# Performance work log

Hardware: AMD Instinct MI355X
Metric: run time of the kernel (lower is better)

## Reference

```python
import jax, jax.numpy as jnp
import numpy as np

# Dimensions: batch B, window W (time features), nodes M, hidden HID, hops NLAYERS
B, W, M, HID, NLAYERS = 32, 168, 2048, 128, 6


def setup_inputs() -> dict:
    key = jax.random.key(0)
    ks = jax.random.split(key, 6)
    x = jax.random.normal(ks[0], (B, W, M), dtype=jnp.float32)
    # scale L so matrix powers L^k stay bounded (spectral radius < 1)
    L = jax.random.normal(ks[1], (M, M), dtype=jnp.float32) / (2.0 * np.float32(np.sqrt(M)))
    # stacked per-hop MLP params: linears[i]: W->HID, linears2[i]: HID->1
    W1 = jax.random.normal(ks[2], (NLAYERS + 1, HID, W), dtype=jnp.float32) / np.float32(np.sqrt(W))
    b1 = jax.random.normal(ks[3], (NLAYERS + 1, HID), dtype=jnp.float32) * 0.01
    W2 = jax.random.normal(ks[4], (NLAYERS + 1, HID), dtype=jnp.float32) / np.float32(np.sqrt(HID))
    b2 = jax.random.normal(ks[5], (NLAYERS + 1,), dtype=jnp.float32) * 0.01
    return {"x": x, "L": L, "W1": W1, "b1": b1, "W2": W2, "b2": b2}


def _hop_mlp(t, w1, bb1, w2, bb2):
    # t: [B, M, W] -> scalar score per node: Linear(W->HID), ReLU, Linear(HID->1)
    h = jax.nn.relu(jnp.einsum('bmw,hw->bmh', t, w1) + bb1)
    return jnp.einsum('bmh,h->bm', h, w2) + bb2


def reference(x, L, W1, b1, W2, b2):
    xt = jnp.swapaxes(x, 1, 2)  # [B, M, W] (x.transpose(2,1))
    s = _hop_mlp(xt, W1[0], b1[0], W2[0], b2[0])  # [B, M]
    P = L
    for i in range(1, NLAYERS + 1):
        # PP.expand + bmm == broadcasted matmul; never materialize [B,M,M]
        t = jnp.einsum('ij,bjw->biw', P, xt)  # [B, M, W]
        s = s + _hop_mlp(t, W1[i], b1[i], W2[i], b2[i])
        P = jnp.matmul(L, P)  # next graph power
    return s  # [B, M]; output_fun is None so no final nonlinearity
```

## Files before the change

### kernel.cpp

```cpp
#include <hip/hip_runtime.h>
#include <cstdint>
#include <cstddef>

typedef __bf16 bf16_t;
typedef __attribute__((ext_vector_type(8))) __bf16 bf16x8;
typedef __attribute__((ext_vector_type(4))) __bf16 bf16x4;
typedef __attribute__((ext_vector_type(4))) float floatx4;

#define NB 32
#define NW 168
#define NM 2048
#define NHID 128
#define NBW (NB * NW)

#define GLOAD_LDS16(g, l)                                          \
  __builtin_amdgcn_global_load_lds(                                \
      (const __attribute__((address_space(1))) void*)(g),          \
      (__attribute__((address_space(3))) void*)(l), 16, 0, 0)

__global__ void cast_bf16_kernel(const float* __restrict__ in, bf16_t* __restrict__ out, int n4) {
  int stride = gridDim.x * blockDim.x;
  for (int i = blockIdx.x * blockDim.x + threadIdx.x; i < n4; i += stride) {
    float4 v = ((const float4*)in)[i];
    bf16x4 o = {(bf16_t)v.x, (bf16_t)v.y, (bf16_t)v.z, (bf16_t)v.w};
    ((bf16x4*)out)[i] = o;
  }
}

__global__ void prep_x_kernel(const float* __restrict__ x, bf16_t* __restrict__ Xb,
                              bf16_t* __restrict__ XT) {
  __shared__ float tile[64][65];
  const int R = NBW, C = NM;
  int r0 = blockIdx.y * 64, c0 = blockIdx.x * 64;
  int t = threadIdx.x;
  int tr = t >> 4, tc4 = (t & 15) * 4;
#pragma unroll
  for (int p = 0; p < 4; ++p) {
    int row = p * 16 + tr;
    float4 v = *(const float4*)(x + (size_t)(r0 + row) * C + c0 + tc4);
    tile[row][tc4 + 0] = v.x;
    tile[row][tc4 + 1] = v.y;
    tile[row][tc4 + 2] = v.z;
    tile[row][tc4 + 3] = v.w;
    bf16x4 o = {(bf16_t)v.x, (bf16_t)v.y, (bf16_t)v.z, (bf16_t)v.w};
    *(bf16x4*)(Xb + (size_t)(r0 + row) * C + c0 + tc4) = o;
  }
  __syncthreads();
#pragma unroll
  for (int p = 0; p < 4; ++p) {
    int c = p * 16 + tr;
    bf16x4 o = {(bf16_t)tile[tc4 + 0][c], (bf16_t)tile[tc4 + 1][c],
                (bf16_t)tile[tc4 + 2][c], (bf16_t)tile[tc4 + 3][c]};
    *(bf16x4*)(XT + (size_t)(c0 + c) * R + r0 + tc4) = o;
  }
}

__global__ void gemm_nt_kernel(const bf16_t* __restrict__ A, const bf16_t* __restrict__ Bt,
                               bf16_t* __restrict__ C, bf16_t* __restrict__ Ct,
                               int K, int lda, int ldb, int ldc, int ldct, int write_c) {
  __shared__ bf16_t As[128 * 32];
  __shared__ bf16_t Bs[128 * 32];
  int tid = threadIdx.x;
  int m0 = blockIdx.y * 128, n0 = blockIdx.x * 128;
  int lane = tid & 63, wv = tid >> 6;
  int wm = wv >> 1, wn = wv & 1;
  int quad = lane >> 4, l15 = lane & 15;

  int p0 = wv * 128 + lane;
  int p1 = p0 + 64;
  int row0 = p0 >> 2, kc0 = (p0 & 3) ^ ((p0 >> 3) & 3);
  int row1 = p1 >> 2, kc1 = (p1 & 3) ^ ((p1 >> 3) & 3);
  const bf16_t* a0p = A + (size_t)(m0 + row0) * lda + kc0 * 8;
  const bf16_t* a1p = A + (size_t)(m0 + row1) * lda + kc1 * 8;
  const bf16_t* b0p = Bt + (size_t)(n0 + row0) * ldb + kc0 * 8;
  const bf16_t* b1p = Bt + (size_t)(n0 + row1) * ldb + kc1 * 8;
  bf16_t* As_d0 = As + (size_t)(wv * 128) * 8;
  bf16_t* As_d1 = As + (size_t)(wv * 128 + 64) * 8;
  bf16_t* Bs_d0 = Bs + (size_t)(wv * 128) * 8;
  bf16_t* Bs_d1 = Bs + (size_t)(wv * 128 + 64) * 8;

  int swz = (l15 >> 1) & 3;
  int kpos = (quad ^ swz) * 8;

  floatx4 zero4 = {0.f, 0.f, 0.f, 0.f};
  floatx4 acc[4][4];
#pragma unroll
  for (int mi = 0; mi < 4; ++mi)
#pragma unroll
    for (int ni = 0; ni < 4; ++ni) acc[mi][ni] = zero4;

  for (int kb = 0; kb < K; kb += 32) {
    GLOAD_LDS16(a0p + kb, As_d0);
    GLOAD_LDS16(a1p + kb, As_d1);
    GLOAD_LDS16(b0p + kb, Bs_d0);
    GLOAD_LDS16(b1p + kb, Bs_d1);
    __syncthreads();
    bf16x8 af[4], bf[4];
#pragma unroll
    for (int mi = 0; mi < 4; ++mi)
      af[mi] = *(const bf16x8*)(As + (wm * 64 + mi * 16 + l15) * 32 + kpos);
#pragma unroll
    for (int ni = 0; ni < 4; ++ni)
      bf[ni] = *(const bf16x8*)(Bs + (wn * 64 + ni * 16 + l15) * 32 + kpos);
#pragma unroll
    for (int mi = 0; mi < 4; ++mi)
#pragma unroll
      for (int ni = 0; ni < 4; ++ni)
        acc[mi][ni] = __builtin_amdgcn_mfma_f32_16x16x32_bf16(af[mi], bf[ni], acc[mi][ni], 0, 0, 0);
    __syncthreads();
  }
#pragma unroll
  for (int mi = 0; mi < 4; ++mi) {
#pragma unroll
    for (int ni = 0; ni < 4; ++ni) {
      int col = n0 + wn * 64 + ni * 16 + l15;
      int rowb = m0 + wm * 64 + mi * 16 + quad * 4;
      bf16x4 tv;
#pragma unroll
      for (int r = 0; r < 4; ++r) tv[r] = (bf16_t)acc[mi][ni][r];
      *(bf16x4*)(Ct + (size_t)col * ldct + rowb) = tv;
      if (write_c) {
#pragma unroll
        for (int r = 0; r < 4; ++r)
          C[(size_t)(rowb + r) * ldc + col] = tv[r];
      }
    }
  }
}

__global__ void mlp_score_kernel(const bf16_t* __restrict__ T, const bf16_t* __restrict__ W1b,
                                 const float* __restrict__ b1, const float* __restrict__ W2,
                                 const float* __restrict__ b2, float* __restrict__ out,
                                 int hop, int accumulate) {
  __shared__ bf16_t Bs[24 * 128 * 8];
  __shared__ float sred[4][64];
  const bf16_t* Wh = W1b + (size_t)hop * NHID * NW;
  const float* b1h = b1 + hop * NHID;
  const float* w2h = W2 + hop * NHID;
  int tid = threadIdx.x;
  int r0 = blockIdx.x * 128;
  int lane = tid & 63, wv = tid >> 6;
  int wm = wv >> 1, wn = wv & 1;
  int quad = lane >> 4, l15 = lane & 15;

  for (int c = 2688 + tid; c < 3072; c += 256) {
    int4 z = {0, 0, 0, 0};
    *(int4*)(Bs + (size_t)c * 8) = z;
  }
  for (int i = 0; i < 11; ++i) {
    int c = i * 256 + tid;
    if (c < 2688) {
      int kc = c >> 7;
      int h = (c & 127) ^ ((kc & 3) << 2);
      GLOAD_LDS16(Wh + (size_t)h * NW + kc * 8, Bs + (size_t)(i * 256 + wv * 64) * 8);
    }
  }

  const bf16_t* arow[4];
#pragma unroll
  for (int mi = 0; mi < 4; ++mi) {
    int R = r0 + wm * 64 + mi * 16 + l15;
    arow[mi] = T + (size_t)(R >> 5) * NBW + (size_t)(R & 31) * NW + quad * 8;
  }

  floatx4 zero4 = {0.f, 0.f, 0.f, 0.f};
  floatx4 acc[4][4];
#pragma unroll
  for (int mi = 0; mi < 4; ++mi)
#pragma unroll
    for (int ni = 0; ni < 4; ++ni) acc[mi][ni] = zero4;

  __syncthreads();

#pragma unroll
  for (int kb = 0; kb < 192; kb += 32) {
    int kc = (kb >> 3) + quad;
    bf16x8 af[4], bf[4];
#pragma unroll
    for (int mi = 0; mi < 4; ++mi)
      af[mi] = *(const bf16x8*)(arow[mi] + kb);
#pragma unroll
    for (int ni = 0; ni < 4; ++ni) {
      int hpos = (wn * 64 + ni * 16 + l15) ^ ((kc & 3) << 2);
      bf[ni] = *(const bf16x8*)(Bs + (size_t)(kc * 128 + hpos) * 8);
    }
#pragma unroll
    for (int mi = 0; mi < 4; ++mi)
#pragma unroll
      for (int ni = 0; ni < 4; ++ni)
        acc[mi][ni] = __builtin_amdgcn_mfma_f32_16x16x32_bf16(af[mi], bf[ni], acc[mi][ni], 0, 0, 0);
  }

  float part[4][4];
#pragma unroll
  for (int mi = 0; mi < 4; ++mi)
#pragma unroll
    for (int r = 0; r < 4; ++r) part[mi][r] = 0.f;
#pragma unroll
  for (int ni = 0; ni < 4; ++ni) {
    int col = wn * 64 + ni * 16 + l15;
    float b1v = b1h[col];
    float w2v = w2h[col];
#pragma unroll
    for (int mi = 0; mi < 4; ++mi)
#pragma unroll
      for (int r = 0; r < 4; ++r) {
        float h = acc[mi][ni][r] + b1v;
        h = h > 0.f ? h : 0.f;
        part[mi][r] += h * w2v;
      }
  }
#pragma unroll
  for (int off = 1; off < 16; off <<= 1)
#pragma unroll
    for (int mi = 0; mi < 4; ++mi)
#pragma unroll
      for (int r = 0; r < 4; ++r) part[mi][r] += __shfl_xor(part[mi][r], off);
  if (l15 == 0) {
#pragma unroll
    for (int mi = 0; mi < 4; ++mi)
#pragma unroll
      for (int r = 0; r < 4; ++r) sred[wv][mi * 16 + quad * 4 + r] = part[mi][r];
  }
  __syncthreads();
  if (tid < 128) {
    int half = tid >> 6;
    int lr = tid & 63;
    float v = sred[half * 2][lr] + sred[half * 2 + 1][lr] + b2[hop];
    int R = r0 + half * 64 + lr;
    int idx = (R & 31) * NM + (R >> 5);
    if (accumulate)
      out[idx] += v;
    else
      out[idx] = v;
  }
}

extern "C" void kernel_launch(void* const* d_in, const int* in_sizes, int n_in,
                              void* d_out, int out_size, void* d_ws, size_t ws_size,
                              hipStream_t stream) {
  const float* x = (const float*)d_in[0];
  const float* L = (const float*)d_in[1];
  const float* W1 = (const float*)d_in[2];
  const float* b1 = (const float*)d_in[3];
  const float* W2 = (const float*)d_in[4];
  const float* b2 = (const float*)d_in[5];
  float* out = (float*)d_out;

  char* ws = (char*)d_ws;
  size_t off = 0;
  auto walloc = [&](size_t bytes) -> void* {
    off = (off + 255) & ~(size_t)255;
    void* p = ws + off;
    off += bytes;
    return p;
  };
  bf16_t* Xb = (bf16_t*)walloc((size_t)NBW * NM * 2);
  bf16_t* XT = (bf16_t*)walloc((size_t)NM * NBW * 2);
  bf16_t* Lb = (bf16_t*)walloc((size_t)NM * NM * 2);
  bf16_t* W1b = (bf16_t*)walloc((size_t)7 * NHID * NW * 2);
  bf16_t* Ta = (bf16_t*)walloc((size_t)NBW * NM * 2);
  (void)ws_size; (void)in_sizes; (void)n_in; (void)out_size;

  prep_x_kernel<<<dim3(NM / 64, NBW / 64), dim3(256), 0, stream>>>(x, Xb, XT);
  cast_bf16_kernel<<<dim3(1024), dim3(256), 0, stream>>>(L, Lb, NM * NM / 4);
  cast_bf16_kernel<<<dim3(64), dim3(256), 0, stream>>>(W1, W1b, 7 * NHID * NW / 4);

  mlp_score_kernel<<<dim3(NM * NB / 128), dim3(256), 0, stream>>>(XT, W1b, b1, W2, b2, out, 0, 0);

  bf16_t* src = Xb;
  bf16_t* dst = Ta;
  for (int i = 1; i <= 6; ++i) {
    gemm_nt_kernel<<<dim3(NM / 128, NBW / 128), dim3(256), 0, stream>>>(
        src, Lb, dst, XT, NM, NM, NM, NM, NBW, (i < 6) ? 1 : 0);
    mlp_score_kernel<<<dim3(NM * NB / 128), dim3(256), 0, stream>>>(XT, W1b, b1, W2, b2, out, i, 1);
    bf16_t* t = src; src = dst; dst = t;
  }
}
```

Measured before the change: 553.3 us.

## Rewrite propagation GEMM with 256x256 tiles and double-buffered async LDS pipeline

The graph-propagation GEMM moves from 128x128 tiles with 256 threads and a single-buffered load/sync loop to 256x256 tiles with 512 threads. Operands are staged in a double-buffered 128KB LDS region via direct global-to-LDS loads, with explicit vmcnt waits, barriers and raised MFMA priority so loads overlap compute. This is meant to hide global latency and raise operand reuse per block. In exchange, the grid shrinks to 168 blocks, fewer than the CU count, and LDS use limits occupancy to one block per CU.

```diff
diff --git a/kernel.cpp b/kernel.cpp
--- a/kernel.cpp
+++ b/kernel.cpp
@@ -55,66 +55,100 @@
   }
 }
 
-__global__ void gemm_nt_kernel(const bf16_t* __restrict__ A, const bf16_t* __restrict__ Bt,
-                               bf16_t* __restrict__ C, bf16_t* __restrict__ Ct,
-                               int K, int lda, int ldb, int ldc, int ldct, int write_c) {
-  __shared__ bf16_t As[128 * 32];
-  __shared__ bf16_t Bs[128 * 32];
-  int tid = threadIdx.x;
-  int m0 = blockIdx.y * 128, n0 = blockIdx.x * 128;
-  int lane = tid & 63, wv = tid >> 6;
-  int wm = wv >> 1, wn = wv & 1;
-  int quad = lane >> 4, l15 = lane & 15;
-
-  int p0 = wv * 128 + lane;
-  int p1 = p0 + 64;
-  int row0 = p0 >> 2, kc0 = (p0 & 3) ^ ((p0 >> 3) & 3);
-  int row1 = p1 >> 2, kc1 = (p1 & 3) ^ ((p1 >> 3) & 3);
-  const bf16_t* a0p = A + (size_t)(m0 + row0) * lda + kc0 * 8;
-  const bf16_t* a1p = A + (size_t)(m0 + row1) * lda + kc1 * 8;
-  const bf16_t* b0p = Bt + (size_t)(n0 + row0) * ldb + kc0 * 8;
-  const bf16_t* b1p = Bt + (size_t)(n0 + row1) * ldb + kc1 * 8;
-  bf16_t* As_d0 = As + (size_t)(wv * 128) * 8;
-  bf16_t* As_d1 = As + (size_t)(wv * 128 + 64) * 8;
-  bf16_t* Bs_d0 = Bs + (size_t)(wv * 128) * 8;
-  bf16_t* Bs_d1 = Bs + (size_t)(wv * 128 + 64) * 8;
-
-  int swz = (l15 >> 1) & 3;
-  int kpos = (quad ^ swz) * 8;
+#define STAGE2(gbase, ld, t, ks, ldsbase)                                        \
+  do {                                                                           \
+    const bf16_t* _g = (gbase) + (size_t)(t) * 64 + (ks) * 32;                   \
+    GLOAD_LDS16(_g, lds + (ldsbase) + (ks) * 8192 + wv * 512);                   \
+    GLOAD_LDS16(_g + (size_t)128 * (ld),                                         \
+                lds + (ldsbase) + (ks) * 8192 + 4096 + wv * 512);                \
+  } while (0)
+
+#define VM4 asm volatile("s_waitcnt vmcnt(4)" ::: "memory")
+
+#define PHASE(bufoff, ks, mh, READB, STG, WAIT)                                  \
+  do {                                                                           \
+    if (READB) {                                                                 \
+      _Pragma("unroll") for (int ni = 0; ni < 4; ++ni)                           \
+          bfr[ni] = *(const bf16x8*)(pB + (bufoff) + (ks) * 8192 + ni * 512);    \
+    }                                                                            \
+    _Pragma("unroll") for (int mi = 0; mi < 4; ++mi)                             \
+        afr[mi] =                                                                \
+            *(const bf16x8*)(pA + (bufoff) + (ks) * 8192 + ((mh) * 4 + mi) * 512); \
+    STG;                                                                         \
+    WAIT;                                                                        \
+    __builtin_amdgcn_s_barrier();                                                \
+    asm volatile("s_waitcnt lgkmcnt(0)" ::: "memory");                           \
+    __builtin_amdgcn_sched_barrier(0);                                           \
+    __builtin_amdgcn_s_setprio(1);                                               \
+    _Pragma("unroll") for (int mi = 0; mi < 4; ++mi)                             \
+        _Pragma("unroll") for (int ni = 0; ni < 4; ++ni)                         \
+            acc[(mh) * 4 + mi][ni] = __builtin_amdgcn_mfma_f32_16x16x32_bf16(    \
+                afr[mi], bfr[ni], acc[(mh) * 4 + mi][ni], 0, 0, 0);              \
+    __builtin_amdgcn_s_setprio(0);                                               \
+    __builtin_amdgcn_s_barrier();                                                \
+  } while (0)
+
+__global__ __launch_bounds__(512, 2) void gemm_nt_kernel(
+    const bf16_t* __restrict__ A, const bf16_t* __restrict__ Bt,
+    bf16_t* __restrict__ C, bf16_t* __restrict__ Ct,
+    int K, int lda, int ldb, int ldc, int ldct, int write_c) {
+  __shared__ bf16_t lds[65536];
+  const int tid = threadIdx.x;
+  const int m0 = blockIdx.y * 256, n0 = blockIdx.x * 256;
+  const int lane = tid & 63, wv = tid >> 6;
+  const int wm = wv >> 2, wn = wv & 3;
+  const int quad = lane >> 4, l15 = lane & 15;
+
+  const int srow = tid >> 2;
+  const int scsw = (tid & 3) ^ (srow & 3);
+  const bf16_t* aS = A + (size_t)(m0 + srow) * lda + scsw * 8;
+  const bf16_t* bS = Bt + (size_t)(n0 + srow) * ldb + scsw * 8;
+
+  const int fsw = (quad ^ (l15 & 3)) * 8;
+  const bf16_t* pA = lds + (size_t)(wm * 128 + l15) * 32 + fsw;
+  const bf16_t* pB = lds + 16384 + (size_t)(wn * 64 + l15) * 32 + fsw;
 
   floatx4 zero4 = {0.f, 0.f, 0.f, 0.f};
-  floatx4 acc[4][4];
-#pragma unroll
-  for (int mi = 0; mi < 4; ++mi)
+  floatx4 acc[8][4];
+#pragma unroll
+  for (int mi = 0; mi < 8; ++mi)
 #pragma unroll
     for (int ni = 0; ni < 4; ++ni) acc[mi][ni] = zero4;
 
-  for (int kb = 0; kb < K; kb += 32) {
-    GLOAD_LDS16(a0p + kb, As_d0);
-    GLOAD_LDS16(a1p + kb, As_d1);
-    GLOAD_LDS16(b0p + kb, Bs_d0);
-    GLOAD_LDS16(b1p + kb, Bs_d1);
-    __syncthreads();
-    bf16x8 af[4], bf[4];
-#pragma unroll
-    for (int mi = 0; mi < 4; ++mi)
-      af[mi] = *(const bf16x8*)(As + (wm * 64 + mi * 16 + l15) * 32 + kpos);
-#pragma unroll
-    for (int ni = 0; ni < 4; ++ni)
-      bf[ni] = *(const bf16x8*)(Bs + (wn * 64 + ni * 16 + l15) * 32 + kpos);
-#pragma unroll
-    for (int mi = 0; mi < 4; ++mi)
-#pragma unroll
-      for (int ni = 0; ni < 4; ++ni)
-        acc[mi][ni] = __builtin_amdgcn_mfma_f32_16x16x32_bf16(af[mi], bf[ni], acc[mi][ni], 0, 0, 0);
-    __syncthreads();
-  }
-#pragma unroll
-  for (int mi = 0; mi < 4; ++mi) {
+  STAGE2(aS, lda, 0, 0, 0);
+  STAGE2(bS, ldb, 0, 0, 16384);
+  STAGE2(aS, lda, 0, 1, 0);
+  STAGE2(bS, ldb, 0, 1, 16384);
+  STAGE2(aS, lda, 1, 0, 32768);
+  STAGE2(bS, ldb, 1, 0, 49152);
+  VM4;
+  __builtin_amdgcn_s_barrier();
+
+  bf16x8 afr[4], bfr[4];
+  const int nt = K >> 6;
+  const int nit = K >> 7;
+#pragma unroll 1
+  for (int i = 0; i < nit; ++i) {
+    const int t1 = 2 * i + 1;
+    const int t2 = (t1 + 1 < nt) ? t1 + 1 : 0;
+    const int t3 = (t1 + 2 < nt) ? t1 + 2 : 0;
+    PHASE(0,     0, 0, 1, STAGE2(aS, lda, t1, 1, 32768), (void)0);
+    PHASE(0,     0, 1, 0, STAGE2(bS, ldb, t1, 1, 49152), (void)0);
+    PHASE(0,     1, 0, 1, STAGE2(aS, lda, t2, 0, 0),     (void)0);
+    PHASE(0,     1, 1, 0, STAGE2(bS, ldb, t2, 0, 16384), VM4);
+    PHASE(32768, 0, 0, 1, STAGE2(aS, lda, t2, 1, 0),     (void)0);
+    PHASE(32768, 0, 1, 0, STAGE2(bS, ldb, t2, 1, 16384), (void)0);
+    PHASE(32768, 1, 0, 1, STAGE2(aS, lda, t3, 0, 32768), (void)0);
+    PHASE(32768, 1, 1, 0, STAGE2(bS, ldb, t3, 0, 49152), VM4);
+  }
+  asm volatile("s_waitcnt vmcnt(0)" ::: "memory");
+
+#pragma unroll
+  for (int mi = 0; mi < 8; ++mi) {
 #pragma unroll
     for (int ni = 0; ni < 4; ++ni) {
       int col = n0 + wn * 64 + ni * 16 + l15;
-      int rowb = m0 + wm * 64 + mi * 16 + quad * 4;
+      int rowb = m0 + wm * 128 + mi * 16 + quad * 4;
       bf16x4 tv;
 #pragma unroll
       for (int r = 0; r < 4; ++r) tv[r] = (bf16_t)acc[mi][ni][r];
@@ -271,7 +305,7 @@
   bf16_t* src = Xb;
   bf16_t* dst = Ta;
   for (int i = 1; i <= 6; ++i) {
-    gemm_nt_kernel<<<dim3(NM / 128, NBW / 128), dim3(256), 0, stream>>>(
+    gemm_nt_kernel<<<dim3(NM / 256, NBW / 256), dim3(512), 0, stream>>>(
         src, Lb, dst, XT, NM, NM, NM, NM, NBW, (i < 6) ? 1 : 0);
     mlp_score_kernel<<<dim3(NM * NB / 128), dim3(256), 0, stream>>>(XT, W1b, b1, W2, b2, out, i, 1);
     bf16_t* t = src; src = dst; dst = t;
```

After: 571.4 us. 1.03x slower.
